# Optimization experiments

Hardware: AMD Instinct MI355X
Metric: run time of the kernel (lower is better)

## Reference

```python
import jax, jax.numpy as jnp
import numpy as np

SCALE = 20.0


def _safe_sqrt(d2):
    # sqrt with zero (sub)gradient at 0, matching torch.norm's behavior at 0
    pos = d2 > 0
    return jnp.sqrt(jnp.where(pos, d2, 1.0)) * pos


def setup_inputs() -> dict:
    key = jax.random.key(0)
    k1, k2, k3 = jax.random.split(key, 3)
    N, L, D, M = 64, 256, 1024, 128
    x = jax.random.normal(k1, (N, L, D), dtype=jnp.float32)
    y = jax.random.normal(k2, (M, D), dtype=jnp.float32)
    attention_mask = jax.random.randint(k3, (N, L), 0, 2, dtype=jnp.int32)
    return {"x": x, "y": y, "attention_mask": attention_mask}


def _ed_calc(x, mask_f):
    # x: [N, L, D], mask_f: [N, L] float
    sq = jnp.sum(x * x, axis=-1)                       # [N, L]
    g = jnp.einsum("nid,njd->nij", x, x)               # [N, L, L]
    d2 = jnp.maximum(sq[:, :, None] + sq[:, None, :] - 2.0 * g, 0.0)
    d = _safe_sqrt(d2)                                 # [N, L, L]
    pair_mask = mask_f[:, :, None] * mask_f[:, None, :]
    ed_sums = jnp.sum(d * pair_mask, axis=(1, 2))
    valid = jnp.clip(jnp.sum(pair_mask, axis=(1, 2)), 1.0, None)
    return ed_sums / valid                             # [N]


def _energy_distance(x, y, mask_f):
    # x: [N, L, D], y: [M, D]
    sqx = jnp.sum(x * x, axis=-1)                      # [N, L]
    sqy = jnp.sum(y * y, axis=-1)                      # [M]
    g = jnp.einsum("nld,md->nml", x, y)                # [N, M, L]
    d2 = jnp.maximum(sqx[:, None, :] + sqy[None, :, None] - 2.0 * g, 0.0)
    d = _safe_sqrt(d2)                                 # [N, M, L]
    d = d * mask_f[:, None, :]
    valid = jnp.clip(jnp.sum(mask_f, axis=1), 1.0, None)  # [N]
    ed_sums = jnp.sum(d, axis=2) / valid[:, None]      # [N, M]
    ed_q = _ed_calc(x, mask_f)                         # [N]
    return 2.0 * ed_sums - ed_q[:, None]               # [N, M]


def reference(x, y, attention_mask):
    mask_f = attention_mask.astype(x.dtype)
    scores = _energy_distance(x, y, mask_f) * SCALE * -1.0  # [N, M]
    n = scores.shape[0]
    logp = jax.nn.log_softmax(scores, axis=-1)
    loss = -jnp.mean(logp[jnp.arange(n), jnp.arange(n)])
    return loss
```

## Files before the change

### kernel.cpp

```cpp
#include <hip/hip_runtime.h>
#include <math.h>

#define N_ 64
#define L_ 256
#define D_ 1024
#define M_ 128
#define BK 64

typedef float f4 __attribute__((ext_vector_type(4)));
typedef short bf16x8 __attribute__((ext_vector_type(8)));
typedef short s8v __attribute__((ext_vector_type(8)));
typedef float f32x4 __attribute__((ext_vector_type(4)));
typedef int i4 __attribute__((ext_vector_type(4)));

__global__ __launch_bounds__(256) void convert_ssq_kernel(const float* __restrict__ x,
                                                          const float* __restrict__ y,
                                                          short* __restrict__ xh,
                                                          short* __restrict__ yh,
                                                          float* __restrict__ sqx,
                                                          float* __restrict__ sqy) {
    int w = threadIdx.x >> 6, lane = threadIdx.x & 63;
    int row = blockIdx.x * 4 + w;
    const float* in;
    short* hi;
    float* ssq;
    int r;
    if (row < N_ * L_) { in = x; hi = xh; ssq = sqx; r = row; }
    else               { in = y; hi = yh; ssq = sqy; r = row - N_ * L_; }
    const f4* p = (const f4*)(in + (size_t)r * D_);
    float s = 0.f;
#pragma unroll
    for (int rep = 0; rep < 2; ++rep) {
        f4 v0 = p[rep * 128 + lane * 2];
        f4 v1 = p[rep * 128 + lane * 2 + 1];
        s8v h;
#pragma unroll
        for (int j = 0; j < 4; ++j) {
            float f = v0[j]; s = fmaf(f, f, s);
            unsigned u = __float_as_uint(f);
            h[j] = (short)((u + 0x7FFFu + ((u >> 16) & 1u)) >> 16);
        }
#pragma unroll
        for (int j = 0; j < 4; ++j) {
            float f = v1[j]; s = fmaf(f, f, s);
            unsigned u = __float_as_uint(f);
            h[4 + j] = (short)((u + 0x7FFFu + ((u >> 16) & 1u)) >> 16);
        }
        *(s8v*)(hi + (size_t)r * D_ + rep * 512 + lane * 8) = h;
    }
#pragma unroll
    for (int off = 32; off; off >>= 1) s += __shfl_down(s, off);
    if (lane == 0) ssq[r] = s;
}

__device__ __forceinline__ int swz(int row, int slot) {
    return (row << 7) + (((slot) ^ (row & 7)) << 4);
}

__device__ __forceinline__ void stage_tile(const short* __restrict__ A,
                                           const short* __restrict__ B,
                                           char* lds, int abase, int bbase,
                                           int k0, int tid) {
    int wofs = (tid >> 6) << 10;
    int r8 = tid >> 3;
    int sl = tid & 7;
#pragma unroll
    for (int i = 0; i < 4; ++i) {
        int row = i * 32 + r8;
        int ss = sl ^ (row & 7);
        __builtin_amdgcn_global_load_lds(
            (const __attribute__((address_space(1))) void*)(A + (size_t)row * D_ + k0 + (ss << 3)),
            (__attribute__((address_space(3))) void*)(lds + abase + (i << 12) + wofs),
            16, 0, 0);
    }
#pragma unroll
    for (int i = 0; i < 2; ++i) {
        int row = i * 32 + r8;
        int ss = sl ^ (row & 7);
        __builtin_amdgcn_global_load_lds(
            (const __attribute__((address_space(1))) void*)(B + (size_t)row * D_ + k0 + (ss << 3)),
            (__attribute__((address_space(3))) void*)(lds + bbase + (i << 12) + wofs),
            16, 0, 0);
    }
}

__device__ __forceinline__ void compute_tile(const char* lds, int abase, int bbase,
                                             int wr, int wc, int fr, int kg,
                                             f32x4 acc[4][2]) {
    bf16x8 a[4][2], b[2][2];
#pragma unroll
    for (int fi = 0; fi < 4; ++fi) {
        int row = (wr << 6) + (fi << 4) + fr;
#pragma unroll
        for (int kh = 0; kh < 2; ++kh)
            a[fi][kh] = *(const bf16x8*)(lds + abase + swz(row, (kh << 2) | kg));
    }
#pragma unroll
    for (int fj = 0; fj < 2; ++fj) {
        int col = (wc << 5) + (fj << 4) + fr;
#pragma unroll
        for (int kh = 0; kh < 2; ++kh)
            b[fj][kh] = *(const bf16x8*)(lds + bbase + swz(col, (kh << 2) | kg));
    }
    __builtin_amdgcn_s_setprio(1);
#pragma unroll
    for (int kh = 0; kh < 2; ++kh)
#pragma unroll
        for (int fi = 0; fi < 4; ++fi)
#pragma unroll
            for (int fj = 0; fj < 2; ++fj)
                acc[fi][fj] = __builtin_amdgcn_mfma_f32_16x16x32_bf16(a[fi][kh], b[fj][kh], acc[fi][fj], 0, 0, 0);
    __builtin_amdgcn_s_setprio(0);
}

__global__ __launch_bounds__(256) void ed_mfma_kernel(
        const short* __restrict__ xh, const short* __restrict__ yh,
        const float* __restrict__ sqx, const float* __restrict__ sqy,
        const int* __restrict__ mask,
        float* __restrict__ ed_raw, float* __restrict__ edq) {
    __shared__ __align__(16) char lds[49152];
    int tid = threadIdx.x;
    int b = blockIdx.x;
    int wid = tid >> 6, lane = tid & 63;
    int wr = wid >> 1, wc = wid & 1;

    int xcd = b & 7;
    int slot = b >> 3;
    int n = xcd * 8 + slot / 12;
    int r = slot % 12;

    int l0, c0, mode;
    const short *Ah, *Bh;
    if (r < 4) {
        mode = 0;
        l0 = (r >> 1) << 7; c0 = (r & 1) << 6;
        Bh = yh + (size_t)c0 * D_;
    } else {
        mode = 1;
        int rr = r - 4;
        l0 = (rr >> 2) << 7; c0 = (rr & 3) << 6;
        Bh = xh + ((size_t)n * L_ + c0) * D_;
    }
    Ah = xh + ((size_t)n * L_ + l0) * D_;

    f32x4 acc[4][2];
#pragma unroll
    for (int i = 0; i < 4; ++i)
#pragma unroll
        for (int j = 0; j < 2; ++j)
            acc[i][j] = (f32x4){0.f, 0.f, 0.f, 0.f};

    int fr = lane & 15, kg = lane >> 4;

    int buf = 0;
    stage_tile(Ah, Bh, lds, 0, 16384, 0, tid);
    for (int t = 0; t < 15; ++t) {
        int nb = buf ^ 1;
        stage_tile(Ah, Bh, lds, nb * 24576, nb * 24576 + 16384, (t + 1) * BK, tid);
        asm volatile("s_waitcnt vmcnt(6)" ::: "memory");
        __builtin_amdgcn_sched_barrier(0);
        __builtin_amdgcn_s_barrier();
        compute_tile(lds, buf * 24576, buf * 24576 + 16384, wr, wc, fr, kg, acc);
        __builtin_amdgcn_sched_barrier(0);
        __builtin_amdgcn_s_barrier();
        buf = nb;
    }
    asm volatile("s_waitcnt vmcnt(0)" ::: "memory");
    __builtin_amdgcn_sched_barrier(0);
    __builtin_amdgcn_s_barrier();
    compute_tile(lds, buf * 24576, buf * 24576 + 16384, wr, wc, fr, kg, acc);

    int rbase = (lane >> 4) << 2;

    if (mode == 0) {
        float sy[2];
#pragma unroll
        for (int fj = 0; fj < 2; ++fj)
            sy[fj] = sqy[c0 + (wc << 5) + (fj << 4) + fr];
        float colsum[2] = {0.f, 0.f};
#pragma unroll
        for (int fi = 0; fi < 4; ++fi) {
#pragma unroll
            for (int rr = 0; rr < 4; ++rr) {
                int gl = l0 + (wr << 6) + (fi << 4) + rbase + rr;
                float sx = sqx[n * L_ + gl];
                float mf = (float)mask[n * L_ + gl];
#pragma unroll
                for (int fj = 0; fj < 2; ++fj) {
                    float raw = fmaf(-2.f, acc[fi][fj][rr], sx + sy[fj]);
                    float dd = raw > 0.f ? sqrtf(raw) : 0.f;
                    colsum[fj] = fmaf(dd, mf, colsum[fj]);
                }
            }
        }
#pragma unroll
        for (int fj = 0; fj < 2; ++fj) {
            colsum[fj] += __shfl_xor(colsum[fj], 16);
            colsum[fj] += __shfl_xor(colsum[fj], 32);
        }
        if (lane < 16) {
#pragma unroll
            for (int fj = 0; fj < 2; ++fj)
                atomicAdd(&ed_raw[n * M_ + c0 + (wc << 5) + (fj << 4) + lane], colsum[fj]);
        }
    } else {
        int gj[2];
        float sj[2], mj[2];
#pragma unroll
        for (int fj = 0; fj < 2; ++fj) {
            gj[fj] = c0 + (wc << 5) + (fj << 4) + fr;
            sj[fj] = sqx[n * L_ + gj[fj]];
            mj[fj] = (float)mask[n * L_ + gj[fj]];
        }
        float tot = 0.f;
#pragma unroll
        for (int fi = 0; fi < 4; ++fi) {
#pragma unroll
            for (int rr = 0; rr < 4; ++rr) {
                int gl = l0 + (wr << 6) + (fi << 4) + rbase + rr;
                float sx = sqx[n * L_ + gl];
                float mf = (float)mask[n * L_ + gl];
#pragma unroll
                for (int fj = 0; fj < 2; ++fj) {
                    float raw = fmaf(-2.f, acc[fi][fj][rr], sx + sj[fj]);
                    float dd = raw > 0.f ? sqrtf(raw) : 0.f;
                    if (gl == gj[fj]) dd = 0.f;
                    tot = fmaf(dd * mf, mj[fj], tot);
                }
            }
        }
#pragma unroll
        for (int off = 32; off; off >>= 1) tot += __shfl_xor(tot, off);
        if (lane == 0) atomicAdd(&edq[n], tot);
    }
}

__global__ __launch_bounds__(256) void score_kernel(const float* __restrict__ ed_raw,
                                                    const float* __restrict__ edq,
                                                    const int* __restrict__ mask,
                                                    float* __restrict__ out) {
    __shared__ float sc[N_ * M_];
    __shared__ float Ssh[N_];
    __shared__ float red[N_];
    int tid = threadIdx.x;
    {
        const i4* mp = (const i4*)(mask + tid * 64);
        int s = 0;
#pragma unroll
        for (int i = 0; i < 16; ++i) { i4 v = mp[i]; s += v[0] + v[1] + v[2] + v[3]; }
        s += __shfl_xor(s, 1);
        s += __shfl_xor(s, 2);
        if ((tid & 3) == 0) Ssh[tid >> 2] = (float)s;
    }
    __syncthreads();
    for (int i = tid; i < N_ * M_; i += 256) {
        int n = i >> 7;
        float Sn = Ssh[n];
        float valid1 = fmaxf(Sn, 1.f);
        float edq_n = edq[n] / fmaxf(Sn * Sn, 1.f);
        sc[i] = -20.f * (2.f * ed_raw[i] / valid1 - edq_n);
    }
    __syncthreads();
    int n = tid >> 2, q = tid & 3;
    const float* row = sc + n * M_;
    float mx = -INFINITY;
    for (int m = q * 32; m < q * 32 + 32; ++m) mx = fmaxf(mx, row[m]);
    mx = fmaxf(mx, __shfl_xor(mx, 1));
    mx = fmaxf(mx, __shfl_xor(mx, 2));
    float se = 0.f;
    for (int m = q * 32; m < q * 32 + 32; ++m) se += expf(row[m] - mx);
    se += __shfl_xor(se, 1);
    se += __shfl_xor(se, 2);
    if (q == 0) red[n] = -(row[n] - mx - logf(se));
    __syncthreads();
    if (tid < 64) {
        float v = red[tid];
#pragma unroll
        for (int off = 32; off; off >>= 1) v += __shfl_down(v, off);
        if (tid == 0) out[0] = v * (1.f / (float)N_);
    }
}

extern "C" void kernel_launch(void* const* d_in, const int* in_sizes, int n_in,
                              void* d_out, int out_size, void* d_ws, size_t ws_size,
                              hipStream_t stream) {
    const float* x = (const float*)d_in[0];
    const float* y = (const float*)d_in[1];
    const int* mask = (const int*)d_in[2];

    char* base = (char*)d_ws;
    float* sqx    = (float*)(base);
    float* sqy    = (float*)(base + 65536);
    float* ed_raw = (float*)(base + 66048);
    float* edq    = (float*)(base + 98816);
    short* xh = (short*)(base + (1 << 20));
    short* yh = xh + 16777216;

    hipMemsetAsync(base + 66048, 0, 33024, stream);

    convert_ssq_kernel<<<(N_ * L_ + M_) / 4, 256, 0, stream>>>(x, y, xh, yh, sqx, sqy);

    ed_mfma_kernel<<<768, 256, 0, stream>>>(xh, yh, sqx, sqy, mask, ed_raw, edq);

    score_kernel<<<1, 256, 0, stream>>>(ed_raw, edq, mask, (float*)d_out);
}
```

Baseline: 140.0 us.

## Fuse memset, convert, MFMA and score kernels into one cooperative persistent kernel

```diff
diff --git a/kernel.cpp b/kernel.cpp
--- a/kernel.cpp
+++ b/kernel.cpp
@@ -1,4 +1,5 @@
 #include <hip/hip_runtime.h>
+#include <hip/hip_cooperative_groups.h>
 #include <math.h>
 
 #define N_ 64
@@ -6,52 +7,14 @@
 #define D_ 1024
 #define M_ 128
 #define BK 64
+#define NJOBS 768
 
 typedef float f4 __attribute__((ext_vector_type(4)));
 typedef short bf16x8 __attribute__((ext_vector_type(8)));
 typedef short s8v __attribute__((ext_vector_type(8)));
 typedef float f32x4 __attribute__((ext_vector_type(4)));
-typedef int i4 __attribute__((ext_vector_type(4)));
-
-__global__ __launch_bounds__(256) void convert_ssq_kernel(const float* __restrict__ x,
-                                                          const float* __restrict__ y,
-                                                          short* __restrict__ xh,
-                                                          short* __restrict__ yh,
-                                                          float* __restrict__ sqx,
-                                                          float* __restrict__ sqy) {
-    int w = threadIdx.x >> 6, lane = threadIdx.x & 63;
-    int row = blockIdx.x * 4 + w;
-    const float* in;
-    short* hi;
-    float* ssq;
-    int r;
-    if (row < N_ * L_) { in = x; hi = xh; ssq = sqx; r = row; }
-    else               { in = y; hi = yh; ssq = sqy; r = row - N_ * L_; }
-    const f4* p = (const f4*)(in + (size_t)r * D_);
-    float s = 0.f;
-#pragma unroll
-    for (int rep = 0; rep < 2; ++rep) {
-        f4 v0 = p[rep * 128 + lane * 2];
-        f4 v1 = p[rep * 128 + lane * 2 + 1];
-        s8v h;
-#pragma unroll
-        for (int j = 0; j < 4; ++j) {
-            float f = v0[j]; s = fmaf(f, f, s);
-            unsigned u = __float_as_uint(f);
-            h[j] = (short)((u + 0x7FFFu + ((u >> 16) & 1u)) >> 16);
-        }
-#pragma unroll
-        for (int j = 0; j < 4; ++j) {
-            float f = v1[j]; s = fmaf(f, f, s);
-            unsigned u = __float_as_uint(f);
-            h[4 + j] = (short)((u + 0x7FFFu + ((u >> 16) & 1u)) >> 16);
-        }
-        *(s8v*)(hi + (size_t)r * D_ + rep * 512 + lane * 8) = h;
-    }
-#pragma unroll
-    for (int off = 32; off; off >>= 1) s += __shfl_down(s, off);
-    if (lane == 0) ssq[r] = s;
-}
+
+namespace cg = cooperative_groups;
 
 __device__ __forceinline__ int swz(int row, int slot) {
     return (row << 7) + (((slot) ^ (row & 7)) << 4);
@@ -113,171 +76,219 @@
     __builtin_amdgcn_s_setprio(0);
 }
 
-__global__ __launch_bounds__(256) void ed_mfma_kernel(
-        const short* __restrict__ xh, const short* __restrict__ yh,
-        const float* __restrict__ sqx, const float* __restrict__ sqy,
+__global__ __launch_bounds__(256, 3) void mega_kernel(
+        const float* __restrict__ x, const float* __restrict__ y,
         const int* __restrict__ mask,
-        float* __restrict__ ed_raw, float* __restrict__ edq) {
+        short* __restrict__ xh, short* __restrict__ yh,
+        float* __restrict__ sqx, float* __restrict__ sqy,
+        float* __restrict__ ed_raw, float* __restrict__ edq,
+        float* __restrict__ out) {
     __shared__ __align__(16) char lds[49152];
     int tid = threadIdx.x;
-    int b = blockIdx.x;
-    int wid = tid >> 6, lane = tid & 63;
-    int wr = wid >> 1, wc = wid & 1;
-
-    int xcd = b & 7;
-    int slot = b >> 3;
-    int n = xcd * 8 + slot / 12;
-    int r = slot % 12;
-
-    int l0, c0, mode;
-    const short *Ah, *Bh;
-    if (r < 4) {
-        mode = 0;
-        l0 = (r >> 1) << 7; c0 = (r & 1) << 6;
-        Bh = yh + (size_t)c0 * D_;
-    } else {
-        mode = 1;
-        int rr = r - 4;
-        l0 = (rr >> 2) << 7; c0 = (rr & 3) << 6;
-        Bh = xh + ((size_t)n * L_ + c0) * D_;
-    }
-    Ah = xh + ((size_t)n * L_ + l0) * D_;
-
-    f32x4 acc[4][2];
-#pragma unroll
-    for (int i = 0; i < 4; ++i)
-#pragma unroll
-        for (int j = 0; j < 2; ++j)
-            acc[i][j] = (f32x4){0.f, 0.f, 0.f, 0.f};
-
-    int fr = lane & 15, kg = lane >> 4;
-
-    int buf = 0;
-    stage_tile(Ah, Bh, lds, 0, 16384, 0, tid);
-    for (int t = 0; t < 15; ++t) {
-        int nb = buf ^ 1;
-        stage_tile(Ah, Bh, lds, nb * 24576, nb * 24576 + 16384, (t + 1) * BK, tid);
-        asm volatile("s_waitcnt vmcnt(6)" ::: "memory");
-        __builtin_amdgcn_sched_barrier(0);
-        __builtin_amdgcn_s_barrier();
-        compute_tile(lds, buf * 24576, buf * 24576 + 16384, wr, wc, fr, kg, acc);
-        __builtin_amdgcn_sched_barrier(0);
-        __builtin_amdgcn_s_barrier();
-        buf = nb;
-    }
-    asm volatile("s_waitcnt vmcnt(0)" ::: "memory");
-    __builtin_amdgcn_sched_barrier(0);
-    __builtin_amdgcn_s_barrier();
-    compute_tile(lds, buf * 24576, buf * 24576 + 16384, wr, wc, fr, kg, acc);
-
-    int rbase = (lane >> 4) << 2;
-
-    if (mode == 0) {
-        float sy[2];
-#pragma unroll
-        for (int fj = 0; fj < 2; ++fj)
-            sy[fj] = sqy[c0 + (wc << 5) + (fj << 4) + fr];
-        float colsum[2] = {0.f, 0.f};
-#pragma unroll
-        for (int fi = 0; fi < 4; ++fi) {
-#pragma unroll
-            for (int rr = 0; rr < 4; ++rr) {
-                int gl = l0 + (wr << 6) + (fi << 4) + rbase + rr;
-                float sx = sqx[n * L_ + gl];
-                float mf = (float)mask[n * L_ + gl];
+    int nb = gridDim.x;
+    cg::grid_group gridg = cg::this_grid();
+
+    if (blockIdx.x == 0) {
+        for (int i = tid; i < N_ * M_ + N_ + 1; i += 256) {
+            if (i < N_ * M_)            ed_raw[i] = 0.f;
+            else if (i < N_ * M_ + N_)  edq[i - N_ * M_] = 0.f;
+            else                        out[0] = 0.f;
+        }
+    }
+
+    {
+        int w = tid >> 6, lane = tid & 63;
+        for (int row = blockIdx.x * 4 + w; row < N_ * L_ + M_; row += nb * 4) {
+            const float* in; short* hi; float* ssq; int r;
+            if (row < N_ * L_) { in = x; hi = xh; ssq = sqx; r = row; }
+            else               { in = y; hi = yh; ssq = sqy; r = row - N_ * L_; }
+            const f4* p = (const f4*)(in + (size_t)r * D_);
+            float s = 0.f;
+#pragma unroll
+            for (int rep = 0; rep < 2; ++rep) {
+                f4 v0 = p[rep * 128 + lane * 2];
+                f4 v1 = p[rep * 128 + lane * 2 + 1];
+                s8v h;
+#pragma unroll
+                for (int j = 0; j < 4; ++j) {
+                    float f = v0[j]; s = fmaf(f, f, s);
+                    unsigned u = __float_as_uint(f);
+                    h[j] = (short)((u + 0x7FFFu + ((u >> 16) & 1u)) >> 16);
+                }
+#pragma unroll
+                for (int j = 0; j < 4; ++j) {
+                    float f = v1[j]; s = fmaf(f, f, s);
+                    unsigned u = __float_as_uint(f);
+                    h[4 + j] = (short)((u + 0x7FFFu + ((u >> 16) & 1u)) >> 16);
+                }
+                *(s8v*)(hi + (size_t)r * D_ + rep * 512 + lane * 8) = h;
+            }
+#pragma unroll
+            for (int off = 32; off; off >>= 1) s += __shfl_down(s, off);
+            if (lane == 0) ssq[r] = s;
+        }
+    }
+
+    gridg.sync();
+
+    {
+        int wid = tid >> 6, lane = tid & 63;
+        int wr = wid >> 1, wc = wid & 1;
+        int fr = lane & 15, kg = lane >> 4;
+
+        for (int job = blockIdx.x; job < NJOBS; job += nb) {
+            __syncthreads();
+
+            int xcd = job & 7;
+            int slot = job >> 3;
+            int n = xcd * 8 + slot / 12;
+            int r = slot % 12;
+
+            int l0, c0, mode;
+            const short *Ah, *Bh;
+            if (r < 4) {
+                mode = 0;
+                l0 = (r >> 1) << 7; c0 = (r & 1) << 6;
+                Bh = yh + (size_t)c0 * D_;
+            } else {
+                mode = 1;
+                int rr = r - 4;
+                l0 = (rr >> 2) << 7; c0 = (rr & 3) << 6;
+                Bh = xh + ((size_t)n * L_ + c0) * D_;
+            }
+            Ah = xh + ((size_t)n * L_ + l0) * D_;
+
+            f32x4 acc[4][2];
+#pragma unroll
+            for (int i = 0; i < 4; ++i)
+#pragma unroll
+                for (int j = 0; j < 2; ++j)
+                    acc[i][j] = (f32x4){0.f, 0.f, 0.f, 0.f};
+
+            int buf = 0;
+            stage_tile(Ah, Bh, lds, 0, 16384, 0, tid);
+            for (int t = 0; t < 15; ++t) {
+                int nbuf = buf ^ 1;
+                stage_tile(Ah, Bh, lds, nbuf * 24576, nbuf * 24576 + 16384, (t + 1) * BK, tid);
+                asm volatile("s_waitcnt vmcnt(6)" ::: "memory");
+                __builtin_amdgcn_sched_barrier(0);
+                __builtin_amdgcn_s_barrier();
+                compute_tile(lds, buf * 24576, buf * 24576 + 16384, wr, wc, fr, kg, acc);
+                __builtin_amdgcn_sched_barrier(0);
+                __builtin_amdgcn_s_barrier();
+                buf = nbuf;
+            }
+            asm volatile("s_waitcnt vmcnt(0)" ::: "memory");
+            __builtin_amdgcn_sched_barrier(0);
+            __builtin_amdgcn_s_barrier();
+            compute_tile(lds, buf * 24576, buf * 24576 + 16384, wr, wc, fr, kg, acc);
+
+            int rbase = (lane >> 4) << 2;
+
+            if (mode == 0) {
+                float sy[2];
+#pragma unroll
+                for (int fj = 0; fj < 2; ++fj)
+                    sy[fj] = sqy[c0 + (wc << 5) + (fj << 4) + fr];
+                float colsum[2] = {0.f, 0.f};
+#pragma unroll
+                for (int fi = 0; fi < 4; ++fi) {
+#pragma unroll
+                    for (int rr = 0; rr < 4; ++rr) {
+                        int gl = l0 + (wr << 6) + (fi << 4) + rbase + rr;
+                        float sx = sqx[n * L_ + gl];
+                        float mf = (float)mask[n * L_ + gl];
+#pragma unroll
+                        for (int fj = 0; fj < 2; ++fj) {
+                            float raw = fmaf(-2.f, acc[fi][fj][rr], sx + sy[fj]);
+                            float dd = raw > 0.f ? sqrtf(raw) : 0.f;
+                            colsum[fj] = fmaf(dd, mf, colsum[fj]);
+                        }
+                    }
+                }
 #pragma unroll
                 for (int fj = 0; fj < 2; ++fj) {
-                    float raw = fmaf(-2.f, acc[fi][fj][rr], sx + sy[fj]);
-                    float dd = raw > 0.f ? sqrtf(raw) : 0.f;
-                    colsum[fj] = fmaf(dd, mf, colsum[fj]);
-                }
+                    colsum[fj] += __shfl_xor(colsum[fj], 16);
+                    colsum[fj] += __shfl_xor(colsum[fj], 32);
+                }
+                if (lane < 16) {
+#pragma unroll
+                    for (int fj = 0; fj < 2; ++fj)
+                        atomicAdd(&ed_raw[n * M_ + c0 + (wc << 5) + (fj << 4) + lane], colsum[fj]);
+                }
+            } else {
+                int gj[2];
+                float sj[2], mj[2];
+#pragma unroll
+                for (int fj = 0; fj < 2; ++fj) {
+                    gj[fj] = c0 + (wc << 5) + (fj << 4) + fr;
+                    sj[fj] = sqx[n * L_ + gj[fj]];
+                    mj[fj] = (float)mask[n * L_ + gj[fj]];
+                }
+                float tot = 0.f;
+#pragma unroll
+                for (int fi = 0; fi < 4; ++fi) {
+#pragma unroll
+                    for (int rr = 0; rr < 4; ++rr) {
+                        int gl = l0 + (wr << 6) + (fi << 4) + rbase + rr;
+                        float sx = sqx[n * L_ + gl];
+                        float mf = (float)mask[n * L_ + gl];
+#pragma unroll
+                        for (int fj = 0; fj < 2; ++fj) {
+                            float raw = fmaf(-2.f, acc[fi][fj][rr], sx + sj[fj]);
+                            float dd = raw > 0.f ? sqrtf(raw) : 0.f;
+                            if (gl == gj[fj]) dd = 0.f;
+                            tot = fmaf(dd * mf, mj[fj], tot);
+                        }
+                    }
+                }
+#pragma unroll
+                for (int off = 32; off; off >>= 1) tot += __shfl_xor(tot, off);
+                if (lane == 0) atomicAdd(&edq[n], tot);
             }
         }
-#pragma unroll
-        for (int fj = 0; fj < 2; ++fj) {
-            colsum[fj] += __shfl_xor(colsum[fj], 16);
-            colsum[fj] += __shfl_xor(colsum[fj], 32);
+    }
+
+    gridg.sync();
+
+    {
+        float* f = (float*)lds;
+        for (int n = blockIdx.x; n < N_; n += nb) {
+            __syncthreads();
+            float sc = 0.f, Sn, mx, se;
+            if (tid < 128) {
+                int s = mask[n * L_ + tid] + mask[n * L_ + 128 + tid];
+#pragma unroll
+                for (int off = 32; off; off >>= 1) s += __shfl_down(s, off);
+                if ((tid & 63) == 0) f[4 + (tid >> 6)] = (float)s;
+            }
+            __syncthreads();
+            Sn = f[4] + f[5];
+            float valid1 = fmaxf(Sn, 1.f);
+            float edq_n = edq[n] / fmaxf(Sn * Sn, 1.f);
+            if (tid < 128) {
+                sc = -20.f * (2.f * ed_raw[n * M_ + tid] / valid1 - edq_n);
+                mx = sc;
+#pragma unroll
+                for (int off = 32; off; off >>= 1) mx = fmaxf(mx, __shfl_xor(mx, off));
+                if ((tid & 63) == 0) f[6 + (tid >> 6)] = mx;
+                if (tid == n) f[8] = sc;
+            }
+            __syncthreads();
+            mx = fmaxf(f[6], f[7]);
+            if (tid < 128) {
+                se = expf(sc - mx);
+#pragma unroll
+                for (int off = 32; off; off >>= 1) se += __shfl_xor(se, off);
+                if ((tid & 63) == 0) f[10 + (tid >> 6)] = se;
+            }
+            __syncthreads();
+            if (tid == 0) {
+                float sesum = f[10] + f[11];
+                float lossn = -(f[8] - mx - logf(sesum));
+                atomicAdd(out, lossn * (1.f / (float)N_));
+            }
         }
-        if (lane < 16) {
-#pragma unroll
-            for (int fj = 0; fj < 2; ++fj)
-                atomicAdd(&ed_raw[n * M_ + c0 + (wc << 5) + (fj << 4) + lane], colsum[fj]);
-        }
-    } else {
-        int gj[2];
-        float sj[2], mj[2];
-#pragma unroll
-        for (int fj = 0; fj < 2; ++fj) {
-            gj[fj] = c0 + (wc << 5) + (fj << 4) + fr;
-            sj[fj] = sqx[n * L_ + gj[fj]];
-            mj[fj] = (float)mask[n * L_ + gj[fj]];
-        }
-        float tot = 0.f;
-#pragma unroll
-        for (int fi = 0; fi < 4; ++fi) {
-#pragma unroll
-            for (int rr = 0; rr < 4; ++rr) {
-                int gl = l0 + (wr << 6) + (fi << 4) + rbase + rr;
-                float sx = sqx[n * L_ + gl];
-                float mf = (float)mask[n * L_ + gl];
-#pragma unroll
-                for (int fj = 0; fj < 2; ++fj) {
-                    float raw = fmaf(-2.f, acc[fi][fj][rr], sx + sj[fj]);
-                    float dd = raw > 0.f ? sqrtf(raw) : 0.f;
-                    if (gl == gj[fj]) dd = 0.f;
-                    tot = fmaf(dd * mf, mj[fj], tot);
-                }
-            }
-        }
-#pragma unroll
-        for (int off = 32; off; off >>= 1) tot += __shfl_xor(tot, off);
-        if (lane == 0) atomicAdd(&edq[n], tot);
-    }
-}
-
-__global__ __launch_bounds__(256) void score_kernel(const float* __restrict__ ed_raw,
-                                                    const float* __restrict__ edq,
-                                                    const int* __restrict__ mask,
-                                                    float* __restrict__ out) {
-    __shared__ float sc[N_ * M_];
-    __shared__ float Ssh[N_];
-    __shared__ float red[N_];
-    int tid = threadIdx.x;
-    {
-        const i4* mp = (const i4*)(mask + tid * 64);
-        int s = 0;
-#pragma unroll
-        for (int i = 0; i < 16; ++i) { i4 v = mp[i]; s += v[0] + v[1] + v[2] + v[3]; }
-        s += __shfl_xor(s, 1);
-        s += __shfl_xor(s, 2);
-        if ((tid & 3) == 0) Ssh[tid >> 2] = (float)s;
-    }
-    __syncthreads();
-    for (int i = tid; i < N_ * M_; i += 256) {
-        int n = i >> 7;
-        float Sn = Ssh[n];
-        float valid1 = fmaxf(Sn, 1.f);
-        float edq_n = edq[n] / fmaxf(Sn * Sn, 1.f);
-        sc[i] = -20.f * (2.f * ed_raw[i] / valid1 - edq_n);
-    }
-    __syncthreads();
-    int n = tid >> 2, q = tid & 3;
-    const float* row = sc + n * M_;
-    float mx = -INFINITY;
-    for (int m = q * 32; m < q * 32 + 32; ++m) mx = fmaxf(mx, row[m]);
-    mx = fmaxf(mx, __shfl_xor(mx, 1));
-    mx = fmaxf(mx, __shfl_xor(mx, 2));
-    float se = 0.f;
-    for (int m = q * 32; m < q * 32 + 32; ++m) se += expf(row[m] - mx);
-    se += __shfl_xor(se, 1);
-    se += __shfl_xor(se, 2);
-    if (q == 0) red[n] = -(row[n] - mx - logf(se));
-    __syncthreads();
-    if (tid < 64) {
-        float v = red[tid];
-#pragma unroll
-        for (int off = 32; off; off >>= 1) v += __shfl_down(v, off);
-        if (tid == 0) out[0] = v * (1.f / (float)N_);
     }
 }
 
@@ -295,12 +306,15 @@
     float* edq    = (float*)(base + 98816);
     short* xh = (short*)(base + (1 << 20));
     short* yh = xh + 16777216;
-
-    hipMemsetAsync(base + 66048, 0, 33024, stream);
-
-    convert_ssq_kernel<<<(N_ * L_ + M_) / 4, 256, 0, stream>>>(x, y, xh, yh, sqx, sqy);
-
-    ed_mfma_kernel<<<768, 256, 0, stream>>>(xh, yh, sqx, sqy, mask, ed_raw, edq);
-
-    score_kernel<<<1, 256, 0, stream>>>(ed_raw, edq, mask, (float*)d_out);
-}
+    float* out = (float*)d_out;
+
+    int maxb = 0;
+    hipOccupancyMaxActiveBlocksPerMultiprocessor(&maxb, mega_kernel, 256, 0);
+    if (maxb < 1) maxb = 1;
+    int grid = maxb * 256;
+    if (grid > NJOBS) grid = NJOBS;
+
+    void* args[] = {(void*)&x, (void*)&y, (void*)&mask, (void*)&xh, (void*)&yh,
+                    (void*)&sqx, (void*)&sqy, (void*)&ed_raw, (void*)&edq, (void*)&out};
+    hipLaunchCooperativeKernel(mega_kernel, dim3(grid), dim3(256), args, 0, stream);
+}
```

Measured after the change: 277.8 us. 98.5% more time.

## Give each wave a private 64x64 tile and double buffer to drop block barriers

Applied to the files above, without the earlier changes.

```diff
diff --git a/kernel.cpp b/kernel.cpp
--- a/kernel.cpp
+++ b/kernel.cpp
@@ -5,7 +5,7 @@
 #define L_ 256
 #define D_ 1024
 #define M_ 128
-#define BK 64
+#define BKW 32
 
 typedef float f4 __attribute__((ext_vector_type(4)));
 typedef short bf16x8 __attribute__((ext_vector_type(8)));
@@ -53,162 +53,142 @@
     if (lane == 0) ssq[r] = s;
 }
 
-__device__ __forceinline__ int swz(int row, int slot) {
-    return (row << 7) + (((slot) ^ (row & 7)) << 4);
-}
-
-__device__ __forceinline__ void stage_tile(const short* __restrict__ A,
-                                           const short* __restrict__ B,
-                                           char* lds, int abase, int bbase,
-                                           int k0, int tid) {
-    int wofs = (tid >> 6) << 10;
-    int r8 = tid >> 3;
-    int sl = tid & 7;
+__device__ __forceinline__ int wswz(int row, int kg) {
+    return (row << 6) + (((kg ^ (row & 3) ^ ((row >> 2) & 3)) & 3) << 4);
+}
+
+__device__ __forceinline__ void wstage(const short* __restrict__ A,
+                                       const short* __restrict__ B,
+                                       char* wlds, int bufofs, int k0, int lane) {
+    int row4 = lane >> 2;
+    int sl = lane & 3;
 #pragma unroll
     for (int i = 0; i < 4; ++i) {
-        int row = i * 32 + r8;
-        int ss = sl ^ (row & 7);
+        int row = (i << 4) + row4;
+        int ss = sl ^ (row & 3) ^ ((row >> 2) & 3);
         __builtin_amdgcn_global_load_lds(
             (const __attribute__((address_space(1))) void*)(A + (size_t)row * D_ + k0 + (ss << 3)),
-            (__attribute__((address_space(3))) void*)(lds + abase + (i << 12) + wofs),
+            (__attribute__((address_space(3))) void*)(wlds + bufofs + (i << 10)),
             16, 0, 0);
     }
 #pragma unroll
-    for (int i = 0; i < 2; ++i) {
-        int row = i * 32 + r8;
-        int ss = sl ^ (row & 7);
+    for (int i = 0; i < 4; ++i) {
+        int row = (i << 4) + row4;
+        int ss = sl ^ (row & 3) ^ ((row >> 2) & 3);
         __builtin_amdgcn_global_load_lds(
             (const __attribute__((address_space(1))) void*)(B + (size_t)row * D_ + k0 + (ss << 3)),
-            (__attribute__((address_space(3))) void*)(lds + bbase + (i << 12) + wofs),
+            (__attribute__((address_space(3))) void*)(wlds + bufofs + 4096 + (i << 10)),
             16, 0, 0);
     }
 }
 
-__device__ __forceinline__ void compute_tile(const char* lds, int abase, int bbase,
-                                             int wr, int wc, int fr, int kg,
-                                             f32x4 acc[4][2]) {
-    bf16x8 a[4][2], b[2][2];
-#pragma unroll
-    for (int fi = 0; fi < 4; ++fi) {
-        int row = (wr << 6) + (fi << 4) + fr;
-#pragma unroll
-        for (int kh = 0; kh < 2; ++kh)
-            a[fi][kh] = *(const bf16x8*)(lds + abase + swz(row, (kh << 2) | kg));
-    }
-#pragma unroll
-    for (int fj = 0; fj < 2; ++fj) {
-        int col = (wc << 5) + (fj << 4) + fr;
-#pragma unroll
-        for (int kh = 0; kh < 2; ++kh)
-            b[fj][kh] = *(const bf16x8*)(lds + bbase + swz(col, (kh << 2) | kg));
-    }
+__device__ __forceinline__ void wcompute(const char* wlds, int bufofs,
+                                         int fr, int kg, f32x4 acc[4][4]) {
+    bf16x8 a[4], b[4];
+#pragma unroll
+    for (int fi = 0; fi < 4; ++fi)
+        a[fi] = *(const bf16x8*)(wlds + bufofs + wswz((fi << 4) + fr, kg));
+#pragma unroll
+    for (int fj = 0; fj < 4; ++fj)
+        b[fj] = *(const bf16x8*)(wlds + bufofs + 4096 + wswz((fj << 4) + fr, kg));
     __builtin_amdgcn_s_setprio(1);
 #pragma unroll
-    for (int kh = 0; kh < 2; ++kh)
-#pragma unroll
-        for (int fi = 0; fi < 4; ++fi)
-#pragma unroll
-            for (int fj = 0; fj < 2; ++fj)
-                acc[fi][fj] = __builtin_amdgcn_mfma_f32_16x16x32_bf16(a[fi][kh], b[fj][kh], acc[fi][fj], 0, 0, 0);
+    for (int fi = 0; fi < 4; ++fi)
+#pragma unroll
+        for (int fj = 0; fj < 4; ++fj)
+            acc[fi][fj] = __builtin_amdgcn_mfma_f32_16x16x32_bf16(a[fi], b[fj], acc[fi][fj], 0, 0, 0);
     __builtin_amdgcn_s_setprio(0);
 }
 
-__global__ __launch_bounds__(256) void ed_mfma_kernel(
+__global__ __launch_bounds__(128) void ed_mfma_kernel(
         const short* __restrict__ xh, const short* __restrict__ yh,
         const float* __restrict__ sqx, const float* __restrict__ sqy,
         const int* __restrict__ mask,
         float* __restrict__ ed_raw, float* __restrict__ edq) {
-    __shared__ __align__(16) char lds[49152];
+    __shared__ __align__(16) char lds[32768];
     int tid = threadIdx.x;
+    int wid = tid >> 6, lane = tid & 63;
+    char* wlds = lds + (wid << 14);
+
     int b = blockIdx.x;
-    int wid = tid >> 6, lane = tid & 63;
-    int wr = wid >> 1, wc = wid & 1;
-
     int xcd = b & 7;
     int slot = b >> 3;
     int n = xcd * 8 + slot / 12;
-    int r = slot % 12;
+    int w = (slot % 12) * 2 + wid;
 
     int l0, c0, mode;
-    const short *Ah, *Bh;
-    if (r < 4) {
+    const short *A, *B;
+    if (w < 8) {
         mode = 0;
-        l0 = (r >> 1) << 7; c0 = (r & 1) << 6;
-        Bh = yh + (size_t)c0 * D_;
+        l0 = (w >> 1) << 6; c0 = (w & 1) << 6;
+        B = yh + (size_t)c0 * D_;
     } else {
         mode = 1;
-        int rr = r - 4;
-        l0 = (rr >> 2) << 7; c0 = (rr & 3) << 6;
-        Bh = xh + ((size_t)n * L_ + c0) * D_;
-    }
-    Ah = xh + ((size_t)n * L_ + l0) * D_;
-
-    f32x4 acc[4][2];
+        int u = w - 8;
+        l0 = (u >> 2) << 6; c0 = (u & 3) << 6;
+        B = xh + ((size_t)n * L_ + c0) * D_;
+    }
+    A = xh + ((size_t)n * L_ + l0) * D_;
+
+    f32x4 acc[4][4];
 #pragma unroll
     for (int i = 0; i < 4; ++i)
 #pragma unroll
-        for (int j = 0; j < 2; ++j)
+        for (int j = 0; j < 4; ++j)
             acc[i][j] = (f32x4){0.f, 0.f, 0.f, 0.f};
 
     int fr = lane & 15, kg = lane >> 4;
 
     int buf = 0;
-    stage_tile(Ah, Bh, lds, 0, 16384, 0, tid);
-    for (int t = 0; t < 15; ++t) {
-        int nb = buf ^ 1;
-        stage_tile(Ah, Bh, lds, nb * 24576, nb * 24576 + 16384, (t + 1) * BK, tid);
-        asm volatile("s_waitcnt vmcnt(6)" ::: "memory");
+    wstage(A, B, wlds, 0, 0, lane);
+    for (int t = 0; t < 31; ++t) {
+        wstage(A, B, wlds, (buf ^ 1) << 13, (t + 1) * BKW, lane);
+        asm volatile("s_waitcnt vmcnt(8)" ::: "memory");
         __builtin_amdgcn_sched_barrier(0);
-        __builtin_amdgcn_s_barrier();
-        compute_tile(lds, buf * 24576, buf * 24576 + 16384, wr, wc, fr, kg, acc);
-        __builtin_amdgcn_sched_barrier(0);
-        __builtin_amdgcn_s_barrier();
-        buf = nb;
+        wcompute(wlds, buf << 13, fr, kg, acc);
+        buf ^= 1;
     }
     asm volatile("s_waitcnt vmcnt(0)" ::: "memory");
     __builtin_amdgcn_sched_barrier(0);
-    __builtin_amdgcn_s_barrier();
-    compute_tile(lds, buf * 24576, buf * 24576 + 16384, wr, wc, fr, kg, acc);
-
-    int rbase = (lane >> 4) << 2;
+    wcompute(wlds, buf << 13, fr, kg, acc);
 
     if (mode == 0) {
-        float sy[2];
-#pragma unroll
-        for (int fj = 0; fj < 2; ++fj)
-            sy[fj] = sqy[c0 + (wc << 5) + (fj << 4) + fr];
-        float colsum[2] = {0.f, 0.f};
+        float sy[4];
+#pragma unroll
+        for (int fj = 0; fj < 4; ++fj)
+            sy[fj] = sqy[c0 + (fj << 4) + fr];
+        float colsum[4] = {0.f, 0.f, 0.f, 0.f};
 #pragma unroll
         for (int fi = 0; fi < 4; ++fi) {
 #pragma unroll
-            for (int rr = 0; rr < 4; ++rr) {
-                int gl = l0 + (wr << 6) + (fi << 4) + rbase + rr;
+            for (int r = 0; r < 4; ++r) {
+                int gl = l0 + (fi << 4) + (kg << 2) + r;
                 float sx = sqx[n * L_ + gl];
                 float mf = (float)mask[n * L_ + gl];
 #pragma unroll
-                for (int fj = 0; fj < 2; ++fj) {
-                    float raw = fmaf(-2.f, acc[fi][fj][rr], sx + sy[fj]);
+                for (int fj = 0; fj < 4; ++fj) {
+                    float raw = fmaf(-2.f, acc[fi][fj][r], sx + sy[fj]);
                     float dd = raw > 0.f ? sqrtf(raw) : 0.f;
                     colsum[fj] = fmaf(dd, mf, colsum[fj]);
                 }
             }
         }
 #pragma unroll
-        for (int fj = 0; fj < 2; ++fj) {
+        for (int fj = 0; fj < 4; ++fj) {
             colsum[fj] += __shfl_xor(colsum[fj], 16);
             colsum[fj] += __shfl_xor(colsum[fj], 32);
         }
         if (lane < 16) {
 #pragma unroll
-            for (int fj = 0; fj < 2; ++fj)
-                atomicAdd(&ed_raw[n * M_ + c0 + (wc << 5) + (fj << 4) + lane], colsum[fj]);
+            for (int fj = 0; fj < 4; ++fj)
+                atomicAdd(&ed_raw[n * M_ + c0 + (fj << 4) + lane], colsum[fj]);
         }
     } else {
-        int gj[2];
-        float sj[2], mj[2];
-#pragma unroll
-        for (int fj = 0; fj < 2; ++fj) {
-            gj[fj] = c0 + (wc << 5) + (fj << 4) + fr;
+        int gj[4];
+        float sj[4], mj[4];
+#pragma unroll
+        for (int fj = 0; fj < 4; ++fj) {
+            gj[fj] = c0 + (fj << 4) + fr;
             sj[fj] = sqx[n * L_ + gj[fj]];
             mj[fj] = (float)mask[n * L_ + gj[fj]];
         }
@@ -216,13 +196,13 @@
 #pragma unroll
         for (int fi = 0; fi < 4; ++fi) {
 #pragma unroll
-            for (int rr = 0; rr < 4; ++rr) {
-                int gl = l0 + (wr << 6) + (fi << 4) + rbase + rr;
+            for (int r = 0; r < 4; ++r) {
+                int gl = l0 + (fi << 4) + (kg << 2) + r;
                 float sx = sqx[n * L_ + gl];
                 float mf = (float)mask[n * L_ + gl];
 #pragma unroll
-                for (int fj = 0; fj < 2; ++fj) {
-                    float raw = fmaf(-2.f, acc[fi][fj][rr], sx + sj[fj]);
+                for (int fj = 0; fj < 4; ++fj) {
+                    float raw = fmaf(-2.f, acc[fi][fj][r], sx + sj[fj]);
                     float dd = raw > 0.f ? sqrtf(raw) : 0.f;
                     if (gl == gj[fj]) dd = 0.f;
                     tot = fmaf(dd * mf, mj[fj], tot);
@@ -300,7 +280,7 @@
 
     convert_ssq_kernel<<<(N_ * L_ + M_) / 4, 256, 0, stream>>>(x, y, xh, yh, sqx, sqy);
 
-    ed_mfma_kernel<<<768, 256, 0, stream>>>(xh, yh, sqx, sqy, mask, ed_raw, edq);
+    ed_mfma_kernel<<<768, 128, 0, stream>>>(xh, yh, sqx, sqy, mask, ed_raw, edq);
 
     score_kernel<<<1, 256, 0, stream>>>(ed_raw, edq, mask, (float*)d_out);
 }
```

New measurement: 143.7 us. +2.7%, slower.
